# Kernel tuning notes

Hardware: AMD Instinct MI355X
Metric: run time of the kernel (lower is better)

## Reference

```python
import jax, jax.numpy as jnp
import numpy as np

NUM_CLASSES = 20
ANCS = np.array([[0.025, 0.033], [0.04, 0.07], [0.08, 0.06], [0.07, 0.15],
                 [0.15, 0.11], [0.14, 0.29], [0.28, 0.22], [0.38, 0.48],
                 [0.9, 0.78]], dtype=np.float32)  # [9,2] (w,h) per anchor, 3 per layer
GRIDS = np.array([52, 26, 13], dtype=np.int32)          # sqrt(NUMS_CENG)
NUMS_CENG = np.array([2704, 676, 169], dtype=np.int32)
CENG_OFF = np.array([0, 2704, 3380], dtype=np.int32)     # cumulative cell offsets
NA = 3                                                    # anchors per layer (NUMS_ANC[0])
DIM_TOTAL = int(NUMS_CENG.sum()) * NA                     # 10647
GDIM = 1 + NUM_CLASSES + 4 + 1 + 4                        # 30
LOSS_WEIGHT = (1.0, 1.0, 1.0, 1.0)
EPS16 = 6.103515625e-05  # torch.finfo(float16).eps
BATCH, NGT = 64, 8


def _match_one(boxes_ltrb, labels):
    """Faithful port of fmatch4yolov3 for one image. boxes_ltrb [G,4], labels [G] int."""
    G = boxes_ltrb.shape[0]
    cxy = (boxes_ltrb[:, :2] + boxes_ltrb[:, 2:]) * 0.5          # [G,2]
    wh = boxes_ltrb[:, 2:] - boxes_ltrb[:, :2]                   # [G,2]
    anc = jnp.asarray(ANCS)                                      # [9,2]
    # IoU of origin-centered (wh-only) boxes vs anchors
    inter = (jnp.minimum(wh[:, None, 0], anc[None, :, 0]) *
             jnp.minimum(wh[:, None, 1], anc[None, :, 1]))       # [G,9]
    iou = inter / (wh.prod(-1)[:, None] + anc.prod(-1)[None, :] - inter)
    ids_p_anc = jnp.argmax(iou, axis=-1)                         # [G] best anchor per GT

    onehot = jax.nn.one_hot(labels - 1, NUM_CLASSES, dtype=boxes_ltrb.dtype)  # [G,C]
    weights = 2.0 - wh.prod(-1)                                  # [G]

    grids_f = jnp.asarray(GRIDS, jnp.float32)                    # [3]
    colrow = (cxy[:, None, :] * grids_f[None, :, None]).astype(jnp.int32)  # [G,3,(col,row)]
    base = (jnp.asarray(CENG_OFF)[None, :]
            + colrow[:, :, 1] * jnp.asarray(GRIDS)[None, :]
            + colrow[:, :, 0]) * NA                              # [G,3] start row per (GT,layer)
    txy = (cxy[:, None, :] - colrow.astype(jnp.float32) / grids_f[None, :, None]) \
          * grids_f[None, :, None]                               # [G,3,2]

    ceng = ids_p_anc // NA                                       # [G] matched layer per GT k
    anc_off = ids_p_anc % NA                                     # [G]
    # writes are over all (i,k) GT pairs, exactly as the original nested loops
    twh = jnp.log(wh[:, None, :] / anc[ids_p_anc][None, :, :])   # [G,G,2] box i / anchor of k
    pos_idx = base[:, ceng] + anc_off[None, :]                   # [G,G]
    txy_sel = txy[:, ceng, :]                                    # [G,G,2]
    val = jnp.concatenate([
        jnp.ones((G, G, 1), boxes_ltrb.dtype),
        jnp.broadcast_to(onehot[:, None, :], (G, G, NUM_CLASSES)),
        txy_sel, twh,
        jnp.broadcast_to(weights[:, None, None], (G, G, 1)),
        jnp.broadcast_to(boxes_ltrb[:, None, :], (G, G, 4)),
    ], axis=-1)                                                  # [G,G,GDIM]

    neg = (base[:, :, None] + jnp.arange(NA)[None, None, :]).reshape(G, 3 * NA)  # [G,9]
    neg_pairs = jnp.broadcast_to(neg[:, None, :], (G, G, 3 * NA)).reshape(G * G, 3 * NA)

    def step(g, x):
        idxn, idxp, v = x
        g = g.at[idxn, 0].set(-1.0)   # mark all 3 anchors of each layer's cell as ignore
        g = g.at[idxp].set(v)         # positive overwrite at matched layer/anchor
        return g, None

    g0 = jnp.zeros((DIM_TOTAL, GDIM), boxes_ltrb.dtype)
    g, _ = jax.lax.scan(step, g0,
                        (neg_pairs, pos_idx.reshape(-1), val.reshape(G * G, GDIM)))
    return g


def _bce_logits(logits, t):
    # BCE(sigmoid(logits), t), numerically stable, same math as x_bce on sigmoid
    return jnp.clip(logits, 0.0) - logits * t + jnp.log1p(jnp.exp(-jnp.abs(logits)))


def _loss(pconf, pcls, ptxywh, gboxes_ltrb, glabels):
    batch = pconf.shape[0]
    gyolos = jax.vmap(_match_one)(gboxes_ltrb, glabels)          # [B,10647,30]
    s_ = 1 + NUM_CLASSES
    gconf = gyolos[:, :, 0]
    mask_pos = (gconf > 0).astype(pconf.dtype)
    mask_neg = (gconf == 0).astype(pconf.dtype)
    nums_pos = jnp.clip(mask_pos.sum(-1), EPS16)

    # cls loss (BCE, positives only)
    gcls = gyolos[:, :, 1:s_]
    l_cls = ((_bce_logits(pcls, gcls).sum(-1) * mask_pos).sum(-1) / nums_pos).mean() \
            * LOSS_WEIGHT[2]

    # conf loss (MSE on sigmoid, separate pos/neg means)
    pconf_sig = jax.nn.sigmoid(pconf).reshape(batch, -1)
    mse = (pconf_sig - gconf) ** 2
    l_conf_pos = (mse * mask_pos).sum() / jnp.clip(mask_pos.sum(), EPS16) * LOSS_WEIGHT[0] * 30
    l_conf_neg = (mse * mask_neg).sum() / jnp.clip(mask_neg.sum(), EPS16) * LOSS_WEIGHT[1] * 30

    # box loss: xy BCE, wh MSE, weighted by (2 - w*h)
    weight = gyolos[:, :, s_ + 4]
    gtxty = gyolos[:, :, s_:s_ + 2]
    gtwth = gyolos[:, :, s_ + 2:s_ + 4]
    l_txty = ((_bce_logits(ptxywh[:, :, :2], gtxty).sum(-1) * mask_pos * weight).sum(-1)
              / nums_pos).mean()
    l_twth = ((((ptxywh[:, :, 2:4] - gtwth) ** 2).sum(-1) * mask_pos * weight).sum(-1)
              / nums_pos).mean()

    return l_conf_pos + l_conf_neg + l_cls + l_txty + l_twth


def setup_inputs() -> dict:
    key = jax.random.key(0)
    k1, k2, k3, k4, k5, k6 = jax.random.split(key, 6)
    pconf = jax.random.normal(k1, (BATCH, DIM_TOTAL, 1), jnp.float32)
    pcls = jax.random.normal(k2, (BATCH, DIM_TOTAL, NUM_CLASSES), jnp.float32)
    ptxywh = jax.random.normal(k3, (BATCH, DIM_TOTAL, 4), jnp.float32)
    cxy = jax.random.uniform(k4, (BATCH, NGT, 2), jnp.float32, 0.2, 0.8)
    wh = jax.random.uniform(k5, (BATCH, NGT, 2), jnp.float32, 0.05, 0.35)
    gboxes_ltrb = jnp.concatenate([cxy - wh / 2, cxy + wh / 2], axis=-1)
    glabels = jax.random.randint(k6, (BATCH, NGT), 1, NUM_CLASSES + 1, jnp.int32)
    return {"pconf": pconf, "pcls": pcls, "ptxywh": ptxywh,
            "gboxes_ltrb": gboxes_ltrb, "glabels": glabels}


def reference(pconf, pcls, ptxywh, gboxes_ltrb, glabels):
    return _loss(pconf, pcls, ptxywh, gboxes_ltrb, glabels)
```

## Files before the change

### kernel.cpp

```cpp
#include <hip/hip_runtime.h>

#define BATCH 64
#define NGT 8
#define DIMT 10647
#define NCLS 20
#define EPS16 6.103515625e-05f

#define WS_CONF_OFF 512
#define NCB 448
#define GRID_A (BATCH + NCB)

__global__ __launch_bounds__(256) void fused_kernel(const float* __restrict__ pconf,
                                                    const float* __restrict__ pcls,
                                                    const float* __restrict__ ptxywh,
                                                    const float* __restrict__ gboxes,
                                                    const int* __restrict__ glabels,
                                                    double* __restrict__ ws)
{
    const int t = threadIdx.x;

    if (blockIdx.x >= BATCH) {
        const int cb = blockIdx.x - BATCH;
        const int n4 = (BATCH * DIMT) / 4;
        const float4* p4 = reinterpret_cast<const float4*>(pconf);
        float acc = 0.0f;
        for (int i = cb * 256 + t; i < n4; i += NCB * 256) {
            float4 v = p4[i];
            float s0 = 1.0f / (1.0f + expf(-v.x));
            float s1 = 1.0f / (1.0f + expf(-v.y));
            float s2 = 1.0f / (1.0f + expf(-v.z));
            float s3 = 1.0f / (1.0f + expf(-v.w));
            acc += s0 * s0 + s1 * s1 + s2 * s2 + s3 * s3;
        }
        for (int off = 32; off > 0; off >>= 1) acc += __shfl_down(acc, off);
        __shared__ float lds[4];
        int wid = t >> 6, lane = t & 63;
        if (lane == 0) lds[wid] = acc;
        __syncthreads();
        if (t == 0) ws[WS_CONF_OFF + cb] = (double)(lds[0] + lds[1] + lds[2] + lds[3]);
        return;
    }

    const int b = blockIdx.x;

    __shared__ int   s_base[NGT][3];
    __shared__ float s_txyx[NGT][3], s_txyy[NGT][3];
    __shared__ float s_w[NGT], s_h[NGT], s_wt[NGT];
    __shared__ int   s_lab[NGT], s_ids[NGT];
    __shared__ int   s_cand[72];

    const float ax[9] = {0.025f, 0.04f, 0.08f, 0.07f, 0.15f, 0.14f, 0.28f, 0.38f, 0.9f};
    const float ay[9] = {0.033f, 0.07f, 0.06f, 0.15f, 0.11f, 0.29f, 0.22f, 0.48f, 0.78f};
    const int grids[3] = {52, 26, 13};
    const int coff[3]  = {0, 2704, 3380};

    if (t < NGT) {
        int i = t;
        float l  = gboxes[(b * NGT + i) * 4 + 0];
        float tp = gboxes[(b * NGT + i) * 4 + 1];
        float r  = gboxes[(b * NGT + i) * 4 + 2];
        float bt = gboxes[(b * NGT + i) * 4 + 3];
        float cx = (l + r) * 0.5f, cy = (tp + bt) * 0.5f;
        float w = r - l, h = bt - tp;
        s_w[i] = w; s_h[i] = h; s_wt[i] = 2.0f - w * h;
        s_lab[i] = glabels[b * NGT + i] - 1;
        float whp = w * h;
        float best = -1.0f; int bi = 0;
        for (int a = 0; a < 9; a++) {
            float inter = fminf(w, ax[a]) * fminf(h, ay[a]);
            float iou = inter / (whp + ax[a] * ay[a] - inter);
            if (iou > best) { best = iou; bi = a; }
        }
        s_ids[i] = bi;
        for (int s = 0; s < 3; s++) {
            float gf = (float)grids[s];
            int col = (int)(cx * gf);
            int row = (int)(cy * gf);
            s_base[i][s] = (coff[s] + row * grids[s] + col) * 3;
            s_txyx[i][s] = (cx - (float)col / gf) * gf;
            s_txyy[i][s] = (cy - (float)row / gf) * gf;
        }
    }
    __syncthreads();

    if (t < 72) {
        int i = t / 9, r = t % 9;
        s_cand[t] = s_base[i][r / 3] + (r % 3);
    }
    __syncthreads();

    float np_loc = 0.f, naff_loc = 0.f, bsig_loc = 0.f, cpos_loc = 0.f;
    float cls_loc = 0.f, txty_loc = 0.f, twth_loc = 0.f;

    if (t < 72) {
        int d = s_cand[t];
        bool canon = true;
        int lastneg_i = -1;
        for (int v = 0; v < 72; ++v) {
            if (s_cand[v] == d) {
                if (v < t) canon = false;
                int iv = v / 9;
                if (iv > lastneg_i) lastneg_i = iv;
            }
        }
        if (canon) {
            naff_loc = 1.0f;
            int negtag = lastneg_i * 16 + 14;
            int best_tag = -1, bi = -1, bj = -1;
            for (int i = 0; i < NGT; i++) {
                for (int j = 0; j < NGT; j++) {
                    int s = s_ids[j] / 3, a = s_ids[j] % 3;
                    int pd = s_base[i][s] + a;
                    if (pd == d) {
                        int tag = i * 16 + j * 2 + 1;
                        if (tag > best_tag) { best_tag = tag; bi = i; bj = j; }
                    }
                }
            }
            float pc = pconf[b * DIMT + d];
            float sg = 1.0f / (1.0f + expf(-pc));
            bsig_loc = sg * sg;
            if (best_tag > negtag) {
                np_loc = 1.0f;
                cpos_loc = (sg - 1.0f) * (sg - 1.0f);
                int lab = s_lab[bi];
                float wt = s_wt[bi];
                int aidx = s_ids[bj];
                int s = aidx / 3;
                float tx = s_txyx[bi][s], ty = s_txyy[bi][s];
                float twx = logf(s_w[bi] / ax[aidx]);
                float twy = logf(s_h[bi] / ay[aidx]);
                const float* pc20 = &pcls[(size_t)(b * DIMT + d) * NCLS];
                float cs = 0.0f;
                for (int c = 0; c < NCLS; c++) {
                    float x = pc20[c];
                    float tt = (c == lab) ? 1.0f : 0.0f;
                    cs += fmaxf(x, 0.0f) - x * tt + log1pf(expf(-fabsf(x)));
                }
                cls_loc = cs;
                const float* pt = &ptxywh[(size_t)(b * DIMT + d) * 4];
                float x0 = pt[0], x1 = pt[1];
                float bce0 = fmaxf(x0, 0.0f) - x0 * tx + log1pf(expf(-fabsf(x0)));
                float bce1 = fmaxf(x1, 0.0f) - x1 * ty + log1pf(expf(-fabsf(x1)));
                txty_loc = (bce0 + bce1) * wt;
                float d2 = (pt[2] - twx) * (pt[2] - twx) + (pt[3] - twy) * (pt[3] - twy);
                twth_loc = d2 * wt;
            }
        }
    }

    for (int off = 32; off > 0; off >>= 1) {
        np_loc   += __shfl_down(np_loc, off);
        naff_loc += __shfl_down(naff_loc, off);
        bsig_loc += __shfl_down(bsig_loc, off);
        cpos_loc += __shfl_down(cpos_loc, off);
        cls_loc  += __shfl_down(cls_loc, off);
        txty_loc += __shfl_down(txty_loc, off);
        twth_loc += __shfl_down(twth_loc, off);
    }
    __shared__ float red[4][7];
    {
        int wid = t >> 6, lane = t & 63;
        if (lane == 0) {
            red[wid][0] = bsig_loc; red[wid][1] = cpos_loc; red[wid][2] = np_loc;
            red[wid][3] = naff_loc; red[wid][4] = cls_loc;  red[wid][5] = txty_loc;
            red[wid][6] = twth_loc;
        }
    }
    __syncthreads();
    if (t == 0) {
        float v[7];
        for (int k = 0; k < 7; k++) v[k] = red[0][k] + red[1][k] + red[2][k] + red[3][k];
        float npos_c = fmaxf(v[2], EPS16);
        ws[b * 8 + 0] = (double)v[0];
        ws[b * 8 + 1] = (double)v[1];
        ws[b * 8 + 2] = (double)v[2];
        ws[b * 8 + 3] = (double)v[3];
        ws[b * 8 + 4] = (double)(v[4] / npos_c);
        ws[b * 8 + 5] = (double)(v[5] / npos_c);
        ws[b * 8 + 6] = (double)(v[6] / npos_c);
    }
}

__global__ __launch_bounds__(512) void final_kernel(const double* __restrict__ ws,
                                                    float* __restrict__ out)
{
    const int t = threadIdx.x;
    double a = (t < NCB) ? ws[WS_CONF_OFF + t] : 0.0;
    for (int off = 32; off > 0; off >>= 1) a += __shfl_down(a, off);
    __shared__ double lds[8];
    if ((t & 63) == 0) lds[t >> 6] = a;
    __syncthreads();

    double v0 = 0, v1 = 0, v2 = 0, v3 = 0, v4 = 0, v5 = 0, v6 = 0;
    if (t < 64) {
        v0 = ws[t * 8 + 0]; v1 = ws[t * 8 + 1]; v2 = ws[t * 8 + 2];
        v3 = ws[t * 8 + 3]; v4 = ws[t * 8 + 4]; v5 = ws[t * 8 + 5];
        v6 = ws[t * 8 + 6];
        for (int off = 32; off > 0; off >>= 1) {
            v0 += __shfl_down(v0, off); v1 += __shfl_down(v1, off);
            v2 += __shfl_down(v2, off); v3 += __shfl_down(v3, off);
            v4 += __shfl_down(v4, off); v5 += __shfl_down(v5, off);
            v6 += __shfl_down(v6, off);
        }
    }
    if (t == 0) {
        double A = lds[0] + lds[1] + lds[2] + lds[3] + lds[4] + lds[5] + lds[6] + lds[7];
        double tot = (double)BATCH * (double)DIMT;
        double lcp  = v1 / fmax(v2, (double)EPS16) * 30.0;
        double lcn  = (A - v0) / fmax(tot - v3, (double)EPS16) * 30.0;
        double lcls  = v4 / (double)BATCH;
        double ltxty = v5 / (double)BATCH;
        double ltwth = v6 / (double)BATCH;
        out[0] = (float)(lcp + lcn + lcls + ltxty + ltwth);
    }
}

extern "C" void kernel_launch(void* const* d_in, const int* in_sizes, int n_in,
                              void* d_out, int out_size, void* d_ws, size_t ws_size,
                              hipStream_t stream)
{
    const float* pconf = (const float*)d_in[0];
    const float* pcls  = (const float*)d_in[1];
    const float* ptxy  = (const float*)d_in[2];
    const float* gbox  = (const float*)d_in[3];
    const int*   glab  = (const int*)d_in[4];
    double* ws = (double*)d_ws;

    fused_kernel<<<GRID_A, 256, 0, stream>>>(pconf, pcls, ptxy, gbox, glab, ws);
    final_kernel<<<1, 512, 0, stream>>>(ws, (float*)d_out);
}
```

Before: 26.59 us.

## Merge final reduction into main kernel via cooperative grid sync

Replaces the two-kernel sequence with a single cooperative launch. Grid-wide sync lets block 0 perform the final reduction, which removes the second kernel launch. The confidence-sum block count drops from 448 to 192 so the whole grid can be co-resident. This adds grid-sync overhead and leaves fewer blocks to stream pconf.

```diff
diff --git a/kernel.cpp b/kernel.cpp
--- a/kernel.cpp
+++ b/kernel.cpp
@@ -1,4 +1,7 @@
 #include <hip/hip_runtime.h>
+#include <hip/hip_cooperative_groups.h>
+
+namespace cg = cooperative_groups;
 
 #define BATCH 64
 #define NGT 8
@@ -7,17 +10,30 @@
 #define EPS16 6.103515625e-05f
 
 #define WS_CONF_OFF 512
-#define NCB 448
-#define GRID_A (BATCH + NCB)
-
-__global__ __launch_bounds__(256) void fused_kernel(const float* __restrict__ pconf,
-                                                    const float* __restrict__ pcls,
-                                                    const float* __restrict__ ptxywh,
-                                                    const float* __restrict__ gboxes,
-                                                    const int* __restrict__ glabels,
-                                                    double* __restrict__ ws)
+#define NCB 192
+#define GRID_TOT (BATCH + NCB)
+
+__global__ __launch_bounds__(256) void fused_all(const float* __restrict__ pconf,
+                                                 const float* __restrict__ pcls,
+                                                 const float* __restrict__ ptxywh,
+                                                 const float* __restrict__ gboxes,
+                                                 const int* __restrict__ glabels,
+                                                 double* __restrict__ ws,
+                                                 float* __restrict__ out)
 {
     const int t = threadIdx.x;
+
+    __shared__ int   s_base[NGT][3];
+    __shared__ float s_txyx[NGT][3], s_txyy[NGT][3];
+    __shared__ float s_w[NGT], s_h[NGT], s_wt[NGT];
+    __shared__ int   s_lab[NGT], s_ids[NGT];
+    __shared__ int   s_cand[72];
+    __shared__ float red[4][7];
+    __shared__ float lds1[4];
+    __shared__ double lds2[4];
+
+    const float ax[9] = {0.025f, 0.04f, 0.08f, 0.07f, 0.15f, 0.14f, 0.28f, 0.38f, 0.9f};
+    const float ay[9] = {0.033f, 0.07f, 0.06f, 0.15f, 0.11f, 0.29f, 0.22f, 0.48f, 0.78f};
 
     if (blockIdx.x >= BATCH) {
         const int cb = blockIdx.x - BATCH;
@@ -33,186 +49,173 @@
             acc += s0 * s0 + s1 * s1 + s2 * s2 + s3 * s3;
         }
         for (int off = 32; off > 0; off >>= 1) acc += __shfl_down(acc, off);
-        __shared__ float lds[4];
         int wid = t >> 6, lane = t & 63;
-        if (lane == 0) lds[wid] = acc;
-        __syncthreads();
-        if (t == 0) ws[WS_CONF_OFF + cb] = (double)(lds[0] + lds[1] + lds[2] + lds[3]);
-        return;
-    }
-
-    const int b = blockIdx.x;
-
-    __shared__ int   s_base[NGT][3];
-    __shared__ float s_txyx[NGT][3], s_txyy[NGT][3];
-    __shared__ float s_w[NGT], s_h[NGT], s_wt[NGT];
-    __shared__ int   s_lab[NGT], s_ids[NGT];
-    __shared__ int   s_cand[72];
-
-    const float ax[9] = {0.025f, 0.04f, 0.08f, 0.07f, 0.15f, 0.14f, 0.28f, 0.38f, 0.9f};
-    const float ay[9] = {0.033f, 0.07f, 0.06f, 0.15f, 0.11f, 0.29f, 0.22f, 0.48f, 0.78f};
-    const int grids[3] = {52, 26, 13};
-    const int coff[3]  = {0, 2704, 3380};
-
-    if (t < NGT) {
-        int i = t;
-        float l  = gboxes[(b * NGT + i) * 4 + 0];
-        float tp = gboxes[(b * NGT + i) * 4 + 1];
-        float r  = gboxes[(b * NGT + i) * 4 + 2];
-        float bt = gboxes[(b * NGT + i) * 4 + 3];
-        float cx = (l + r) * 0.5f, cy = (tp + bt) * 0.5f;
-        float w = r - l, h = bt - tp;
-        s_w[i] = w; s_h[i] = h; s_wt[i] = 2.0f - w * h;
-        s_lab[i] = glabels[b * NGT + i] - 1;
-        float whp = w * h;
-        float best = -1.0f; int bi = 0;
-        for (int a = 0; a < 9; a++) {
-            float inter = fminf(w, ax[a]) * fminf(h, ay[a]);
-            float iou = inter / (whp + ax[a] * ay[a] - inter);
-            if (iou > best) { best = iou; bi = a; }
-        }
-        s_ids[i] = bi;
-        for (int s = 0; s < 3; s++) {
-            float gf = (float)grids[s];
-            int col = (int)(cx * gf);
-            int row = (int)(cy * gf);
-            s_base[i][s] = (coff[s] + row * grids[s] + col) * 3;
-            s_txyx[i][s] = (cx - (float)col / gf) * gf;
-            s_txyy[i][s] = (cy - (float)row / gf) * gf;
-        }
-    }
-    __syncthreads();
-
-    if (t < 72) {
-        int i = t / 9, r = t % 9;
-        s_cand[t] = s_base[i][r / 3] + (r % 3);
-    }
-    __syncthreads();
-
-    float np_loc = 0.f, naff_loc = 0.f, bsig_loc = 0.f, cpos_loc = 0.f;
-    float cls_loc = 0.f, txty_loc = 0.f, twth_loc = 0.f;
-
-    if (t < 72) {
-        int d = s_cand[t];
-        bool canon = true;
-        int lastneg_i = -1;
-        for (int v = 0; v < 72; ++v) {
-            if (s_cand[v] == d) {
-                if (v < t) canon = false;
-                int iv = v / 9;
-                if (iv > lastneg_i) lastneg_i = iv;
-            }
-        }
-        if (canon) {
-            naff_loc = 1.0f;
-            int negtag = lastneg_i * 16 + 14;
-            int best_tag = -1, bi = -1, bj = -1;
-            for (int i = 0; i < NGT; i++) {
-                for (int j = 0; j < NGT; j++) {
-                    int s = s_ids[j] / 3, a = s_ids[j] % 3;
-                    int pd = s_base[i][s] + a;
-                    if (pd == d) {
-                        int tag = i * 16 + j * 2 + 1;
-                        if (tag > best_tag) { best_tag = tag; bi = i; bj = j; }
+        if (lane == 0) lds1[wid] = acc;
+        __syncthreads();
+        if (t == 0) ws[WS_CONF_OFF + cb] = (double)(lds1[0] + lds1[1] + lds1[2] + lds1[3]);
+    } else {
+        const int b = blockIdx.x;
+        const int grids[3] = {52, 26, 13};
+        const int coff[3]  = {0, 2704, 3380};
+
+        if (t < NGT) {
+            int i = t;
+            float l  = gboxes[(b * NGT + i) * 4 + 0];
+            float tp = gboxes[(b * NGT + i) * 4 + 1];
+            float r  = gboxes[(b * NGT + i) * 4 + 2];
+            float bt = gboxes[(b * NGT + i) * 4 + 3];
+            float cx = (l + r) * 0.5f, cy = (tp + bt) * 0.5f;
+            float w = r - l, h = bt - tp;
+            s_w[i] = w; s_h[i] = h; s_wt[i] = 2.0f - w * h;
+            s_lab[i] = glabels[b * NGT + i] - 1;
+            float whp = w * h;
+            float best = -1.0f; int bi = 0;
+            for (int a = 0; a < 9; a++) {
+                float inter = fminf(w, ax[a]) * fminf(h, ay[a]);
+                float iou = inter / (whp + ax[a] * ay[a] - inter);
+                if (iou > best) { best = iou; bi = a; }
+            }
+            s_ids[i] = bi;
+            for (int s = 0; s < 3; s++) {
+                float gf = (float)grids[s];
+                int col = (int)(cx * gf);
+                int row = (int)(cy * gf);
+                s_base[i][s] = (coff[s] + row * grids[s] + col) * 3;
+                s_txyx[i][s] = (cx - (float)col / gf) * gf;
+                s_txyy[i][s] = (cy - (float)row / gf) * gf;
+            }
+        }
+        __syncthreads();
+
+        if (t < 72) {
+            int i = t / 9, r = t % 9;
+            s_cand[t] = s_base[i][r / 3] + (r % 3);
+        }
+        __syncthreads();
+
+        float np_loc = 0.f, naff_loc = 0.f, bsig_loc = 0.f, cpos_loc = 0.f;
+        float cls_loc = 0.f, txty_loc = 0.f, twth_loc = 0.f;
+
+        if (t < 72) {
+            int d = s_cand[t];
+            bool canon = true;
+            int lastneg_i = -1;
+            for (int v = 0; v < 72; ++v) {
+                if (s_cand[v] == d) {
+                    if (v < t) canon = false;
+                    int iv = v / 9;
+                    if (iv > lastneg_i) lastneg_i = iv;
+                }
+            }
+            if (canon) {
+                naff_loc = 1.0f;
+                int negtag = lastneg_i * 16 + 14;
+                int best_tag = -1, bi = -1, bj = -1;
+                for (int i = 0; i < NGT; i++) {
+                    for (int j = 0; j < NGT; j++) {
+                        int s = s_ids[j] / 3, a = s_ids[j] % 3;
+                        int pd = s_base[i][s] + a;
+                        if (pd == d) {
+                            int tag = i * 16 + j * 2 + 1;
+                            if (tag > best_tag) { best_tag = tag; bi = i; bj = j; }
+                        }
                     }
                 }
-            }
-            float pc = pconf[b * DIMT + d];
-            float sg = 1.0f / (1.0f + expf(-pc));
-            bsig_loc = sg * sg;
-            if (best_tag > negtag) {
-                np_loc = 1.0f;
-                cpos_loc = (sg - 1.0f) * (sg - 1.0f);
-                int lab = s_lab[bi];
-                float wt = s_wt[bi];
-                int aidx = s_ids[bj];
-                int s = aidx / 3;
-                float tx = s_txyx[bi][s], ty = s_txyy[bi][s];
-                float twx = logf(s_w[bi] / ax[aidx]);
-                float twy = logf(s_h[bi] / ay[aidx]);
-                const float* pc20 = &pcls[(size_t)(b * DIMT + d) * NCLS];
-                float cs = 0.0f;
-                for (int c = 0; c < NCLS; c++) {
-                    float x = pc20[c];
-                    float tt = (c == lab) ? 1.0f : 0.0f;
-                    cs += fmaxf(x, 0.0f) - x * tt + log1pf(expf(-fabsf(x)));
+                float pc = pconf[b * DIMT + d];
+                float sg = 1.0f / (1.0f + expf(-pc));
+                bsig_loc = sg * sg;
+                if (best_tag > negtag) {
+                    np_loc = 1.0f;
+                    cpos_loc = (sg - 1.0f) * (sg - 1.0f);
+                    int lab = s_lab[bi];
+                    float wt = s_wt[bi];
+                    int aidx = s_ids[bj];
+                    int s = aidx / 3;
+                    float tx = s_txyx[bi][s], ty = s_txyy[bi][s];
+                    float twx = logf(s_w[bi] / ax[aidx]);
+                    float twy = logf(s_h[bi] / ay[aidx]);
+                    const float* pc20 = &pcls[(size_t)(b * DIMT + d) * NCLS];
+                    float cs = 0.0f;
+                    for (int c = 0; c < NCLS; c++) {
+                        float x = pc20[c];
+                        float tt = (c == lab) ? 1.0f : 0.0f;
+                        cs += fmaxf(x, 0.0f) - x * tt + log1pf(expf(-fabsf(x)));
+                    }
+                    cls_loc = cs;
+                    const float* pt = &ptxywh[(size_t)(b * DIMT + d) * 4];
+                    float x0 = pt[0], x1 = pt[1];
+                    float bce0 = fmaxf(x0, 0.0f) - x0 * tx + log1pf(expf(-fabsf(x0)));
+                    float bce1 = fmaxf(x1, 0.0f) - x1 * ty + log1pf(expf(-fabsf(x1)));
+                    txty_loc = (bce0 + bce1) * wt;
+                    float d2 = (pt[2] - twx) * (pt[2] - twx) + (pt[3] - twy) * (pt[3] - twy);
+                    twth_loc = d2 * wt;
                 }
-                cls_loc = cs;
-                const float* pt = &ptxywh[(size_t)(b * DIMT + d) * 4];
-                float x0 = pt[0], x1 = pt[1];
-                float bce0 = fmaxf(x0, 0.0f) - x0 * tx + log1pf(expf(-fabsf(x0)));
-                float bce1 = fmaxf(x1, 0.0f) - x1 * ty + log1pf(expf(-fabsf(x1)));
-                txty_loc = (bce0 + bce1) * wt;
-                float d2 = (pt[2] - twx) * (pt[2] - twx) + (pt[3] - twy) * (pt[3] - twy);
-                twth_loc = d2 * wt;
-            }
+            }
+        }
+
+        for (int off = 32; off > 0; off >>= 1) {
+            np_loc   += __shfl_down(np_loc, off);
+            naff_loc += __shfl_down(naff_loc, off);
+            bsig_loc += __shfl_down(bsig_loc, off);
+            cpos_loc += __shfl_down(cpos_loc, off);
+            cls_loc  += __shfl_down(cls_loc, off);
+            txty_loc += __shfl_down(txty_loc, off);
+            twth_loc += __shfl_down(twth_loc, off);
+        }
+        {
+            int wid = t >> 6, lane = t & 63;
+            if (lane == 0) {
+                red[wid][0] = bsig_loc; red[wid][1] = cpos_loc; red[wid][2] = np_loc;
+                red[wid][3] = naff_loc; red[wid][4] = cls_loc;  red[wid][5] = txty_loc;
+                red[wid][6] = twth_loc;
+            }
+        }
+        __syncthreads();
+        if (t == 0) {
+            float v[7];
+            for (int k = 0; k < 7; k++) v[k] = red[0][k] + red[1][k] + red[2][k] + red[3][k];
+            float npos_c = fmaxf(v[2], EPS16);
+            ws[b * 8 + 0] = (double)v[0];
+            ws[b * 8 + 1] = (double)v[1];
+            ws[b * 8 + 2] = (double)v[2];
+            ws[b * 8 + 3] = (double)v[3];
+            ws[b * 8 + 4] = (double)(v[4] / npos_c);
+            ws[b * 8 + 5] = (double)(v[5] / npos_c);
+            ws[b * 8 + 6] = (double)(v[6] / npos_c);
         }
     }
 
-    for (int off = 32; off > 0; off >>= 1) {
-        np_loc   += __shfl_down(np_loc, off);
-        naff_loc += __shfl_down(naff_loc, off);
-        bsig_loc += __shfl_down(bsig_loc, off);
-        cpos_loc += __shfl_down(cpos_loc, off);
-        cls_loc  += __shfl_down(cls_loc, off);
-        txty_loc += __shfl_down(txty_loc, off);
-        twth_loc += __shfl_down(twth_loc, off);
-    }
-    __shared__ float red[4][7];
-    {
-        int wid = t >> 6, lane = t & 63;
-        if (lane == 0) {
-            red[wid][0] = bsig_loc; red[wid][1] = cpos_loc; red[wid][2] = np_loc;
-            red[wid][3] = naff_loc; red[wid][4] = cls_loc;  red[wid][5] = txty_loc;
-            red[wid][6] = twth_loc;
-        }
-    }
-    __syncthreads();
-    if (t == 0) {
-        float v[7];
-        for (int k = 0; k < 7; k++) v[k] = red[0][k] + red[1][k] + red[2][k] + red[3][k];
-        float npos_c = fmaxf(v[2], EPS16);
-        ws[b * 8 + 0] = (double)v[0];
-        ws[b * 8 + 1] = (double)v[1];
-        ws[b * 8 + 2] = (double)v[2];
-        ws[b * 8 + 3] = (double)v[3];
-        ws[b * 8 + 4] = (double)(v[4] / npos_c);
-        ws[b * 8 + 5] = (double)(v[5] / npos_c);
-        ws[b * 8 + 6] = (double)(v[6] / npos_c);
-    }
-}
-
-__global__ __launch_bounds__(512) void final_kernel(const double* __restrict__ ws,
-                                                    float* __restrict__ out)
-{
-    const int t = threadIdx.x;
-    double a = (t < NCB) ? ws[WS_CONF_OFF + t] : 0.0;
-    for (int off = 32; off > 0; off >>= 1) a += __shfl_down(a, off);
-    __shared__ double lds[8];
-    if ((t & 63) == 0) lds[t >> 6] = a;
-    __syncthreads();
-
-    double v0 = 0, v1 = 0, v2 = 0, v3 = 0, v4 = 0, v5 = 0, v6 = 0;
-    if (t < 64) {
-        v0 = ws[t * 8 + 0]; v1 = ws[t * 8 + 1]; v2 = ws[t * 8 + 2];
-        v3 = ws[t * 8 + 3]; v4 = ws[t * 8 + 4]; v5 = ws[t * 8 + 5];
-        v6 = ws[t * 8 + 6];
-        for (int off = 32; off > 0; off >>= 1) {
-            v0 += __shfl_down(v0, off); v1 += __shfl_down(v1, off);
-            v2 += __shfl_down(v2, off); v3 += __shfl_down(v3, off);
-            v4 += __shfl_down(v4, off); v5 += __shfl_down(v5, off);
-            v6 += __shfl_down(v6, off);
-        }
-    }
-    if (t == 0) {
-        double A = lds[0] + lds[1] + lds[2] + lds[3] + lds[4] + lds[5] + lds[6] + lds[7];
-        double tot = (double)BATCH * (double)DIMT;
-        double lcp  = v1 / fmax(v2, (double)EPS16) * 30.0;
-        double lcn  = (A - v0) / fmax(tot - v3, (double)EPS16) * 30.0;
-        double lcls  = v4 / (double)BATCH;
-        double ltxty = v5 / (double)BATCH;
-        double ltwth = v6 / (double)BATCH;
-        out[0] = (float)(lcp + lcn + lcls + ltxty + ltwth);
+    __threadfence();
+    cg::this_grid().sync();
+
+    if (blockIdx.x == 0) {
+        double a = (t < NCB) ? ws[WS_CONF_OFF + t] : 0.0;
+        for (int off = 32; off > 0; off >>= 1) a += __shfl_down(a, off);
+        if ((t & 63) == 0) lds2[t >> 6] = a;
+        __syncthreads();
+
+        double v0 = 0, v1 = 0, v2 = 0, v3 = 0, v4 = 0, v5 = 0, v6 = 0;
+        if (t < 64) {
+            v0 = ws[t * 8 + 0]; v1 = ws[t * 8 + 1]; v2 = ws[t * 8 + 2];
+            v3 = ws[t * 8 + 3]; v4 = ws[t * 8 + 4]; v5 = ws[t * 8 + 5];
+            v6 = ws[t * 8 + 6];
+            for (int off = 32; off > 0; off >>= 1) {
+                v0 += __shfl_down(v0, off); v1 += __shfl_down(v1, off);
+                v2 += __shfl_down(v2, off); v3 += __shfl_down(v3, off);
+                v4 += __shfl_down(v4, off); v5 += __shfl_down(v5, off);
+                v6 += __shfl_down(v6, off);
+            }
+        }
+        if (t == 0) {
+            double A = lds2[0] + lds2[1] + lds2[2] + lds2[3];
+            double tot = (double)BATCH * (double)DIMT;
+            double lcp  = v1 / fmax(v2, (double)EPS16) * 30.0;
+            double lcn  = (A - v0) / fmax(tot - v3, (double)EPS16) * 30.0;
+            double lcls  = v4 / (double)BATCH;
+            double ltxty = v5 / (double)BATCH;
+            double ltwth = v6 / (double)BATCH;
+            out[0] = (float)(lcp + lcn + lcls + ltxty + ltwth);
+        }
     }
 }
 
@@ -226,7 +229,10 @@
     const float* gbox  = (const float*)d_in[3];
     const int*   glab  = (const int*)d_in[4];
     double* ws = (double*)d_ws;
-
-    fused_kernel<<<GRID_A, 256, 0, stream>>>(pconf, pcls, ptxy, gbox, glab, ws);
-    final_kernel<<<1, 512, 0, stream>>>(ws, (float*)d_out);
+    float* outp = (float*)d_out;
+
+    void* args[] = {(void*)&pconf, (void*)&pcls, (void*)&ptxy, (void*)&gbox,
+                    (void*)&glab, (void*)&ws, (void*)&outp};
+    hipLaunchCooperativeKernel((const void*)fused_all, dim3(GRID_TOT), dim3(256),
+                               args, 0, stream);
 }
```

After: 80.58 us. +203.1%, slower.
